# Performance work log

Measured on AMD Instinct MI355X. Metric: run time of the kernel, lower is better.

Reference implementation:

```python
import jax, jax.numpy as jnp
import numpy as np
from itertools import permutations

B, T, S = 32, 65536, 4
EPS = 1e-7
PIT_W, VAD_W = 1.0, 0.5
PERMS = np.array(list(permutations(range(S))), dtype=np.int32)  # [24, 4]


def setup_inputs() -> dict:
    key = jax.random.key(0)
    k1, k2, k3, k4, k5 = jax.random.split(key, 5)
    pred_speakers = jax.random.uniform(k1, (B, T, S), dtype=jnp.float32)
    pred_vad = jax.random.uniform(k2, (B, T), dtype=jnp.float32)
    labels = jax.random.randint(k3, (B, T, S), 0, 2).astype(jnp.float32)
    vad = jax.random.randint(k4, (B, T), 0, 2).astype(jnp.float32)
    lengths = jnp.maximum(jax.random.randint(k5, (B,), 0, T), T // 2).astype(jnp.int64)
    return {"pred_speakers": pred_speakers, "pred_vad": pred_vad,
            "labels": labels, "vad": vad, "lengths": lengths}


def reference(pred_speakers, pred_vad, labels, vad, lengths):
    mask = (jnp.arange(T)[None, :] < lengths[:, None]).astype(jnp.float32)  # [B,T]
    msum = mask.sum(axis=1)  # [B]

    # --- PIT speaker loss (num_speakers=4 -> exact permutation search) ---
    p = jnp.clip(pred_speakers, EPS, 1.0 - EPS)
    lp = jnp.log(p)          # log p
    lq = jnp.log1p(-p)       # log(1-p)
    # pairwise masked BCE cost: L[b,i,j] = sum_t mask * bce(pred_i, target_j) / sum_t mask
    #   bce = -(t*lp + (1-t)*lq) = -t*(lp-lq) - lq
    mt = labels * mask[:, :, None]                              # [B,T,S]
    term1 = -jnp.einsum('bti,btj->bij', lp - lq, mt)            # [B,S,S]
    term2 = -(lq * mask[:, :, None]).sum(axis=1)                # [B,S]
    L = (term1 + term2[:, :, None]) / msum[:, None, None]       # [B,S,S]
    perms = jnp.asarray(PERMS)                                  # [24,S]
    # perm_loss[b,p] = mean_i L[b, i, perms[p,i]]
    perm_losses = L[:, jnp.arange(S)[None, :], perms].mean(axis=-1)  # [B,24]
    speaker_loss = perm_losses.min(axis=1).mean()

    # --- VAD BCE loss ---
    pv = jnp.clip(pred_vad, EPS, 1.0 - EPS)
    bce_v = -(vad * jnp.log(pv) + (1.0 - vad) * jnp.log1p(-pv))
    vad_loss = (bce_v * mask).sum() / mask.sum()

    return PIT_W * speaker_loss + VAD_W * vad_loss
```

## Files before the change

### kernel.cpp

```cpp
#include <hip/hip_runtime.h>

#define B 32
#define T 65536
#define EPSF 1e-7f
#define TPB 256
#define CHUNK 2048
#define NCHUNKB (T / CHUNK)
#define NBLK (B * NCHUNKB)
#define NACC 21
#define NCOL (B * NACC)

__device__ __forceinline__ float wave_reduce_sum(float v) {
    #pragma unroll
    for (int off = 32; off > 0; off >>= 1) v += __shfl_down(v, off, 64);
    return v;
}

__device__ __forceinline__ void accum_sp(float4 p4, float4 l4,
                                         float (&a1)[16], float (&a2)[4]) {
    const float p[4] = {p4.x, p4.y, p4.z, p4.w};
    const float l[4] = {l4.x, l4.y, l4.z, l4.w};
    float d[4];
    #pragma unroll
    for (int i = 0; i < 4; ++i) {
        const float pc = fminf(fmaxf(p[i], EPSF), 1.0f - EPSF);
        const float lp = __logf(pc);
        const float lq = __logf(1.0f - pc);
        a2[i] += lq;
        d[i] = lp - lq;
    }
    #pragma unroll
    for (int i = 0; i < 4; ++i)
        #pragma unroll
        for (int j = 0; j < 4; ++j)
            a1[i * 4 + j] = fmaf(d[i], l[j], a1[i * 4 + j]);
}

__device__ __forceinline__ void accum_vad1(float pvv, float vdd, float& av) {
    const float pvc = fminf(fmaxf(pvv, EPSF), 1.0f - EPSF);
    av += __logf((vdd > 0.5f) ? pvc : (1.0f - pvc));
}

__device__ __forceinline__ void accum_vad4(float4 v4, float4 w4, float& av) {
    accum_vad1(v4.x, w4.x, av);
    accum_vad1(v4.y, w4.y, av);
    accum_vad1(v4.z, w4.z, av);
    accum_vad1(v4.w, w4.w, av);
}

__global__ __launch_bounds__(TPB) void partial_kernel(
    const float4* __restrict__ ps,
    const float*  __restrict__ pv,
    const float4* __restrict__ lb,
    const float*  __restrict__ vd,
    const int*    __restrict__ len,
    float* __restrict__ part)
{
    const int b  = blockIdx.x >> 5;
    const int c  = blockIdx.x & (NCHUNKB - 1);
    const int t0 = c * CHUNK;
    const int L  = len[b];
    const int tid = threadIdx.x;

    float a1[16], a2[4], av = 0.0f;
    #pragma unroll
    for (int k = 0; k < 16; ++k) a1[k] = 0.0f;
    #pragma unroll
    for (int k = 0; k < 4; ++k)  a2[k] = 0.0f;

    if (t0 < L) {
        if (t0 + CHUNK <= L) {
            const int base = b * T + t0 + tid;

            float4 P0[4], Q0[4];
            #pragma unroll
            for (int u = 0; u < 4; ++u) {
                const int g = base + u * TPB;
                P0[u] = ps[g];  Q0[u] = lb[g];
            }
            const int gv = b * T + t0 + tid * 8;
            const float4 V0 = *reinterpret_cast<const float4*>(pv + gv);
            const float4 V1 = *reinterpret_cast<const float4*>(pv + gv + 4);
            const float4 W0 = *reinterpret_cast<const float4*>(vd + gv);
            const float4 W1 = *reinterpret_cast<const float4*>(vd + gv + 4);

            #pragma unroll
            for (int u = 0; u < 4; ++u)
                accum_sp(P0[u], Q0[u], a1, a2);

            float4 P1[4], Q1[4];
            #pragma unroll
            for (int u = 0; u < 4; ++u) {
                const int g = base + (4 + u) * TPB;
                P1[u] = ps[g];  Q1[u] = lb[g];
            }
            #pragma unroll
            for (int u = 0; u < 4; ++u)
                accum_sp(P1[u], Q1[u], a1, a2);

            accum_vad4(V0, W0, av);
            accum_vad4(V1, W1, av);
        } else {
            #pragma unroll
            for (int u = 0; u < 8; ++u) {
                const int t = t0 + tid + u * TPB;
                if (t < L) {
                    const int g = b * T + t;
                    const float4 p4 = ps[g];
                    const float4 l4 = lb[g];
                    accum_sp(p4, l4, a1, a2);
                    accum_vad1(pv[g], vd[g], av);
                }
            }
        }
    }

    __shared__ float smem[TPB / 64][NACC];
    const int lane = tid & 63;
    const int wv   = tid >> 6;

    float vals[NACC];
    #pragma unroll
    for (int k = 0; k < 16; ++k) vals[k] = a1[k];
    #pragma unroll
    for (int k = 0; k < 4; ++k)  vals[16 + k] = a2[k];
    vals[20] = av;

    #pragma unroll
    for (int k = 0; k < NACC; ++k) {
        const float r = wave_reduce_sum(vals[k]);
        if (lane == 0) smem[wv][k] = r;
    }
    __syncthreads();
    if (tid < NACC) {
        float s = 0.0f;
        #pragma unroll
        for (int w = 0; w < TPB / 64; ++w) s += smem[w][tid];
        part[c * NCOL + b * NACC + tid] = s;
    }
}

__global__ __launch_bounds__(704) void final_kernel(
    const float* __restrict__ part,
    const int*   __restrict__ len,
    float* __restrict__ out)
{
    __shared__ float sums[B][NACC];
    const int tid = threadIdx.x;

    if (tid < NCOL) {
        float a = 0.0f;
        #pragma unroll
        for (int c = 0; c < NCHUNKB; ++c)
            a += part[c * NCOL + tid];
        sums[tid / NACC][tid % NACC] = a;
    }
    __syncthreads();

    if (tid < 64) {
        float best = 0.0f, vadn = 0.0f, lensum = 0.0f;
        if (tid < B) {
            const int bb = tid;
            const float msum = (float)len[bb];
            float Lm[16];
            #pragma unroll
            for (int i = 0; i < 4; ++i)
                #pragma unroll
                for (int j = 0; j < 4; ++j)
                    Lm[i * 4 + j] = (-sums[bb][i * 4 + j] - sums[bb][16 + i]) / msum;

            best = 1e30f;
            #pragma unroll
            for (int p0 = 0; p0 < 4; ++p0)
                #pragma unroll
                for (int p1 = 0; p1 < 4; ++p1) {
                    if (p1 == p0) continue;
                    #pragma unroll
                    for (int p2 = 0; p2 < 4; ++p2) {
                        if (p2 == p0 || p2 == p1) continue;
                        const int p3 = 6 - p0 - p1 - p2;
                        best = fminf(best, Lm[p0] + Lm[4 + p1] + Lm[8 + p2] + Lm[12 + p3]);
                    }
                }
            best *= 0.25f;
            vadn   = -sums[bb][20];
            lensum = msum;
        }
        best   = wave_reduce_sum(best);
        vadn   = wave_reduce_sum(vadn);
        lensum = wave_reduce_sum(lensum);
        if (tid == 0)
            out[0] = best * (1.0f / B) + 0.5f * (vadn / lensum);
    }
}

extern "C" void kernel_launch(void* const* d_in, const int* in_sizes, int n_in,
                              void* d_out, int out_size, void* d_ws, size_t ws_size,
                              hipStream_t stream) {
    const float4* ps  = (const float4*)d_in[0];
    const float*  pv  = (const float*)d_in[1];
    const float4* lb  = (const float4*)d_in[2];
    const float*  vd  = (const float*)d_in[3];
    const int*    len = (const int*)d_in[4];
    float*        part = (float*)d_ws;
    float*        out  = (float*)d_out;

    partial_kernel<<<NBLK, TPB, 0, stream>>>(ps, pv, lb, vd, len, part);
    final_kernel<<<1, 704, 0, stream>>>(part, len, out);
}
```

Measured before the change: 115.3 us.

## Fuse final reduction into partial kernel via atomics and last-block counter

Replaces the two-kernel scheme with one kernel. Each block atomically adds its 21 partial sums into global accumulators, then bumps a completion counter, and the last block to finish computes the PIT minimum and VAD loss. This removes the second kernel launch and the partial-buffer round trip. In exchange it adds a memset launch, 21 float atomics per block that contend on the same addresses, and a float summation order that varies from run to run.

```diff
diff --git a/kernel.cpp b/kernel.cpp
--- a/kernel.cpp
+++ b/kernel.cpp
@@ -48,13 +48,15 @@
     accum_vad1(v4.w, w4.w, av);
 }
 
-__global__ __launch_bounds__(TPB) void partial_kernel(
+__global__ __launch_bounds__(TPB) void fused_kernel(
     const float4* __restrict__ ps,
     const float*  __restrict__ pv,
     const float4* __restrict__ lb,
     const float*  __restrict__ vd,
     const int*    __restrict__ len,
-    float* __restrict__ part)
+    float* __restrict__ sums_g,
+    int*   __restrict__ counter,
+    float* __restrict__ out)
 {
     const int b  = blockIdx.x >> 5;
     const int c  = blockIdx.x & (NCHUNKB - 1);
@@ -116,6 +118,7 @@
     }
 
     __shared__ float smem[TPB / 64][NACC];
+    __shared__ int s_last;
     const int lane = tid & 63;
     const int wv   = tid >> 6;
 
@@ -132,28 +135,28 @@
         if (lane == 0) smem[wv][k] = r;
     }
     __syncthreads();
+
     if (tid < NACC) {
         float s = 0.0f;
         #pragma unroll
         for (int w = 0; w < TPB / 64; ++w) s += smem[w][tid];
-        part[c * NCOL + b * NACC + tid] = s;
-    }
-}
-
-__global__ __launch_bounds__(704) void final_kernel(
-    const float* __restrict__ part,
-    const int*   __restrict__ len,
-    float* __restrict__ out)
-{
+        atomicAdd(&sums_g[b * NACC + tid], s);
+    }
+    __syncthreads();
+    if (tid == 0) {
+        const int old = __hip_atomic_fetch_add(counter, 1, __ATOMIC_ACQ_REL,
+                                               __HIP_MEMORY_SCOPE_AGENT);
+        s_last = (old == NBLK - 1) ? 1 : 0;
+    }
+    __syncthreads();
+    if (!s_last) return;
+
+    __threadfence();
     __shared__ float sums[B][NACC];
-    const int tid = threadIdx.x;
-
-    if (tid < NCOL) {
-        float a = 0.0f;
-        #pragma unroll
-        for (int c = 0; c < NCHUNKB; ++c)
-            a += part[c * NCOL + tid];
-        sums[tid / NACC][tid % NACC] = a;
+    for (int col = tid; col < NCOL; col += TPB) {
+        const float v = __hip_atomic_load(&sums_g[col], __ATOMIC_RELAXED,
+                                          __HIP_MEMORY_SCOPE_AGENT);
+        sums[col / NACC][col % NACC] = v;
     }
     __syncthreads();
 
@@ -202,9 +205,13 @@
     const float4* lb  = (const float4*)d_in[2];
     const float*  vd  = (const float*)d_in[3];
     const int*    len = (const int*)d_in[4];
-    float*        part = (float*)d_ws;
+    float*        sums_g  = (float*)d_ws;
+    int*          counter = (int*)((float*)d_ws + NCOL);
     float*        out  = (float*)d_out;
 
-    partial_kernel<<<NBLK, TPB, 0, stream>>>(ps, pv, lb, vd, len, part);
-    final_kernel<<<1, 704, 0, stream>>>(part, len, out);
-}
+    hipMemsetAsync(d_ws, 0, (NCOL + 1) * sizeof(float), stream);
+
+    void* kp0 = (void*)ps;
+    (void)kp0;
+    fused_kernel<<<NBLK, TPB, 0, stream>>>(ps, pv, lb, vd, len, sums_g, counter, out);
+}
```

Result: slower. 146.5 us (+27.1%).
